# Performance work log

Measured on AMD Instinct MI355X. Metric: run time of the kernel, lower is better.

## Reference

```python
import jax, jax.numpy as jnp
import numpy as np
import math

D_MODEL = 1024
NUM_HEADS = 16
D_FF = 4096
LN_EPS = 1e-5


def _layer_norm(x, gamma, beta):
    mu = jnp.mean(x, axis=-1, keepdims=True)
    var = jnp.mean(jnp.square(x - mu), axis=-1, keepdims=True)
    return (x - mu) / jnp.sqrt(var + LN_EPS) * gamma + beta


def setup_inputs() -> dict:
    key = jax.random.key(0)
    ks = jax.random.split(key, 16)
    S, B, D, F = 2048, 2, D_MODEL, D_FF
    sc = 0.02
    inp = {
        "x": jax.random.normal(ks[0], (S, B, D), dtype=jnp.float32),
        "Wq": jax.random.normal(ks[1], (D, D), dtype=jnp.float32) * sc,
        "bq": jnp.zeros((D,), jnp.float32),
        "Wk": jax.random.normal(ks[2], (D, D), dtype=jnp.float32) * sc,
        "bk": jnp.zeros((D,), jnp.float32),
        "Wv": jax.random.normal(ks[3], (D, D), dtype=jnp.float32) * sc,
        "bv": jnp.zeros((D,), jnp.float32),
        "Wo": jax.random.normal(ks[4], (D, D), dtype=jnp.float32) * sc,
        "bo": jnp.zeros((D,), jnp.float32),
        "g1": jnp.ones((D,), jnp.float32),
        "b1": jnp.zeros((D,), jnp.float32),
        "W1": jax.random.normal(ks[5], (D, F), dtype=jnp.float32) * sc,
        "bb1": jnp.zeros((F,), jnp.float32),
        "W2": jax.random.normal(ks[6], (F, D), dtype=jnp.float32) * sc,
        "bb2": jnp.zeros((D,), jnp.float32),
        "g2": jnp.ones((D,), jnp.float32),
        "b2": jnp.zeros((D,), jnp.float32),
    }
    return inp


def reference(x, Wq, bq, Wk, bk, Wv, bv, Wo, bo, g1, b1, W1, bb1, W2, bb2, g2, b2):
    # x: [S, B, D] (seq-first, matching the torch module)
    S, B, D = x.shape
    H = NUM_HEADS
    dh = D // H

    def split_(t):  # [S, B, D] -> [B*H, S, dh]  (same as view + transpose in torch)
        return jnp.swapaxes(t.reshape(S, B * H, dh), 0, 1)

    q = split_(x @ Wq + bq)
    k = split_(x @ Wk + bk)
    v = split_(x @ Wv + bv)

    # naive bmm -> softmax -> bmm attention (full [B*H, S, S] scores)
    scores = jnp.einsum("nsd,ntd->nst", q / math.sqrt(dh), k)
    attn = jax.nn.softmax(scores, axis=-1)
    o = jnp.einsum("nst,ntd->nsd", attn, v)  # [B*H, S, dh]
    o = jnp.swapaxes(o, 0, 1).reshape(S, B, D) @ Wo + bo

    x1 = _layer_norm(x + o, g1, b1)
    ff = jax.nn.relu(x1 @ W1 + bb1) @ W2 + bb2
    return _layer_norm(x1 + ff, g2, b2)
```

## Files before the change

kernel.cpp:

```cpp
#include <hip/hip_runtime.h>
#include <hip/hip_bf16.h>
#include <cstdint>

typedef __bf16 bf16_t;
typedef __attribute__((ext_vector_type(8))) __bf16 bf16x8;
typedef __attribute__((ext_vector_type(4))) __bf16 bf16x4;
typedef __attribute__((ext_vector_type(2))) __bf16 bf16x2;
typedef __attribute__((ext_vector_type(4))) float f32x4;

#define GLOBAL_AS __attribute__((address_space(1)))
#define LDS_AS __attribute__((address_space(3)))

__device__ __forceinline__ void lds_load16(void* lds, const void* g) {
    __builtin_amdgcn_global_load_lds((GLOBAL_AS void*)g, (LDS_AS void*)lds, 16, 0, 0);
}

__global__ __launch_bounds__(256) void cast_f32_bf16(const float* __restrict__ in,
                                                     bf16_t* __restrict__ out, int n4) {
    int i = (blockIdx.x * 256 + threadIdx.x);
    if (i >= n4) return;
    float4 v = *(const float4*)(in + (size_t)i * 4);
    bf16x4 o;
    o[0] = (bf16_t)v.x; o[1] = (bf16_t)v.y; o[2] = (bf16_t)v.z; o[3] = (bf16_t)v.w;
    *(bf16x4*)(out + (size_t)i * 4) = o;
}

__global__ __launch_bounds__(256) void transpose_cast(const float* __restrict__ W,
                                                      bf16_t* __restrict__ WT,
                                                      int Kd, int Nd) {
    __shared__ float T[64][65];
    const int nbk = Kd >> 6;
    const int bk = blockIdx.x % nbk, bn = blockIdx.x / nbk;
    const int k0 = bk << 6, n0 = bn << 6;
    const int tid = threadIdx.x;
    #pragma unroll
    for (int rep = 0; rep < 4; ++rep) {
        int r = rep * 16 + (tid >> 4);
        int c = (tid & 15) * 4;
        float4 v = *(const float4*)(W + (size_t)(k0 + r) * Nd + n0 + c);
        T[r][c] = v.x; T[r][c + 1] = v.y; T[r][c + 2] = v.z; T[r][c + 3] = v.w;
    }
    __syncthreads();
    #pragma unroll
    for (int rep = 0; rep < 4; ++rep) {
        int r = rep * 16 + (tid >> 4);
        int c = (tid & 15) * 4;
        bf16x4 o;
        o[0] = (bf16_t)T[c][r]; o[1] = (bf16_t)T[c + 1][r];
        o[2] = (bf16_t)T[c + 2][r]; o[3] = (bf16_t)T[c + 3][r];
        *(bf16x4*)(WT + (size_t)(n0 + r) * Kd + k0 + c) = o;
    }
}

__global__ __launch_bounds__(256) void concat_bias(const float* a, const float* b,
                                                   const float* c, float* o) {
    int i = blockIdx.x * 256 + threadIdx.x;
    o[i] = (i < 1024) ? a[i] : (i < 2048) ? b[i - 1024] : c[i - 2048];
}

template <int OM , bool RELU>
__global__ __launch_bounds__(512, 2) void gemm256(const bf16_t* __restrict__ A,
                                                  const bf16_t* __restrict__ Bt,
                                                  const float* __restrict__ bias,
                                                  void* __restrict__ Cv,
                                                  int M, int N, int K,
                                                  int kc_len, int n_kc) {
    __shared__ alignas(16) bf16_t As[2][256 * 64];
    __shared__ alignas(16) bf16_t Bs[2][256 * 64];
    const int tid = threadIdx.x;
    const int wid = tid >> 6, lane = tid & 63;
    const int lr = lane & 15, lg = lane >> 4;
    const int wr = wid >> 2, wc = wid & 3;
    const int lrsw = (lr & 7) << 4;

    const int nbn = N >> 8;
    const int nbase = (M >> 8) * nbn;
    const int nwg = nbase * n_kc;
    int bid = blockIdx.x;
    int wg;
    if ((nwg & 7) == 0) { int q = nwg >> 3; wg = (bid & 7) * q + (bid >> 3); }
    else wg = bid;
    const int kc = wg / nbase;
    const int inner = wg - kc * nbase;
    const int bm = inner / nbn, bn = inner % nbn;

    f32x4 acc[8][4];
    #pragma unroll
    for (int i = 0; i < 8; ++i)
        #pragma unroll
        for (int j = 0; j < 4; ++j) acc[i][j] = f32x4{0.f, 0.f, 0.f, 0.f};

    const int srow = wid * 16 + (lane >> 3);
    const int colbyte = (((lane & 7) ^ (lane >> 3)) << 4);
    const char* gA = (const char*)(A + ((size_t)(bm * 256 + srow) * K + kc * kc_len)) + colbyte;
    const char* gB = (const char*)(Bt + ((size_t)(bn * 256 + srow) * K + kc * kc_len)) + colbyte;
    const size_t rs8 = (size_t)8 * K * 2;
    const size_t rs128 = (size_t)128 * K * 2;

    auto stA = [&](int b, int half, int kt) {
        char* d = (char*)As[b] + (half * 128 + wid * 16) * 128;
        const char* s = gA + (size_t)half * rs128 + (size_t)kt * 128;
        lds_load16(d, s);
        lds_load16(d + 1024, s + rs8);
    };
    auto stB = [&](int b, int half, int kt) {
        char* d = (char*)Bs[b] + (half * 128 + wid * 16) * 128;
        const char* s = gB + (size_t)half * rs128 + (size_t)kt * 128;
        lds_load16(d, s);
        lds_load16(d + 1024, s + rs8);
    };
    auto ldA = [&](int b, int m, int kk) {
        const int row = (m >> 2) * 128 + (m & 3) * 32 + wr * 16 + lr;
        return *(const bf16x8*)((const char*)As[b] + row * 128 + ((kk * 64 + lg * 16) ^ lrsw));
    };
    auto ldB = [&](int b, int n, int kk) {
        const int row = n * 64 + wc * 16 + lr;
        return *(const bf16x8*)((const char*)Bs[b] + row * 128 + ((kk * 64 + lg * 16) ^ lrsw));
    };

    const int NT = kc_len >> 6;
    stA(0, 0, 0); stB(0, 0, 0); stB(0, 1, 0); stA(0, 1, 0);
    asm volatile("s_waitcnt vmcnt(4)" ::: "memory");
    __builtin_amdgcn_s_barrier();

    bf16x8 afr[4][2], bfr[4][2];
    #pragma unroll 1
    for (int kt = 0; kt < NT; ++kt) {
        const int buf = kt & 1;
        const int ktn = (kt + 1 < NT) ? kt + 1 : kt;

        #pragma unroll
        for (int m = 0; m < 4; ++m) {
            afr[m][0] = ldA(buf, m, 0);
            afr[m][1] = ldA(buf, m, 1);
        }
        #pragma unroll
        for (int n = 0; n < 2; ++n) {
            bfr[n][0] = ldB(buf, n, 0);
            bfr[n][1] = ldB(buf, n, 1);
        }
        stA(buf ^ 1, 0, ktn);
        __builtin_amdgcn_s_barrier();
        __builtin_amdgcn_s_setprio(1);
        #pragma unroll
        for (int m = 0; m < 4; ++m)
            #pragma unroll
            for (int n = 0; n < 2; ++n) {
                acc[m][n] = __builtin_amdgcn_mfma_f32_16x16x32_bf16(afr[m][0], bfr[n][0], acc[m][n], 0, 0, 0);
                acc[m][n] = __builtin_amdgcn_mfma_f32_16x16x32_bf16(afr[m][1], bfr[n][1], acc[m][n], 0, 0, 0);
            }
        __builtin_amdgcn_s_setprio(0);
        asm volatile("s_waitcnt vmcnt(4)" ::: "memory");
        __builtin_amdgcn_s_barrier();

        #pragma unroll
        for (int n = 2; n < 4; ++n) {
            bfr[n][0] = ldB(buf, n, 0);
            bfr[n][1] = ldB(buf, n, 1);
        }
        stB(buf ^ 1, 0, ktn);
        __builtin_amdgcn_s_barrier();
        __builtin_amdgcn_s_setprio(1);
        #pragma unroll
        for (int m = 0; m < 4; ++m)
            #pragma unroll
            for (int n = 2; n < 4; ++n) {
                acc[m][n] = __builtin_amdgcn_mfma_f32_16x16x32_bf16(afr[m][0], bfr[n][0], acc[m][n], 0, 0, 0);
                acc[m][n] = __builtin_amdgcn_mfma_f32_16x16x32_bf16(afr[m][1], bfr[n][1], acc[m][n], 0, 0, 0);
            }
        __builtin_amdgcn_s_setprio(0);
        asm volatile("s_waitcnt vmcnt(4)" ::: "memory");
        __builtin_amdgcn_s_barrier();

        #pragma unroll
        for (int m = 0; m < 4; ++m) {
            afr[m][0] = ldA(buf, m + 4, 0);
            afr[m][1] = ldA(buf, m + 4, 1);
        }
        stB(buf ^ 1, 1, ktn);
        __builtin_amdgcn_s_barrier();
        __builtin_amdgcn_s_setprio(1);
        #pragma unroll
        for (int m = 0; m < 4; ++m)
            #pragma unroll
            for (int n = 0; n < 2; ++n) {
                acc[m + 4][n] = __builtin_amdgcn_mfma_f32_16x16x32_bf16(afr[m][0], bfr[n][0], acc[m + 4][n], 0, 0, 0);
                acc[m + 4][n] = __builtin_amdgcn_mfma_f32_16x16x32_bf16(afr[m][1], bfr[n][1], acc[m + 4][n], 0, 0, 0);
            }
        __builtin_amdgcn_s_setprio(0);
        __builtin_amdgcn_s_barrier();

        stA(buf ^ 1, 1, ktn);
        __builtin_amdgcn_s_barrier();
        __builtin_amdgcn_s_setprio(1);
        #pragma unroll
        for (int m = 0; m < 4; ++m)
            #pragma unroll
            for (int n = 2; n < 4; ++n) {
                acc[m + 4][n] = __builtin_amdgcn_mfma_f32_16x16x32_bf16(afr[m][0], bfr[n][0], acc[m + 4][n], 0, 0, 0);
                acc[m + 4][n] = __builtin_amdgcn_mfma_f32_16x16x32_bf16(afr[m][1], bfr[n][1], acc[m + 4][n], 0, 0, 0);
            }
        __builtin_amdgcn_s_setprio(0);
        asm volatile("s_waitcnt vmcnt(4)" ::: "memory");
        __builtin_amdgcn_s_barrier();
    }

    float* outp = (float*)Cv + (size_t)kc * M * N;
    float bv[4];
    #pragma unroll
    for (int n = 0; n < 4; ++n) {
        const int c = (bn << 8) + n * 64 + wc * 16 + lr;
        bv[n] = (bias && kc == 0) ? bias[c] : 0.f;
    }
    #pragma unroll
    for (int m = 0; m < 8; ++m) {
        const int row0 = (bm << 8) + (m >> 2) * 128 + (m & 3) * 32 + wr * 16 + (lg << 2);
        #pragma unroll
        for (int n = 0; n < 4; ++n) {
            const int c = (bn << 8) + n * 64 + wc * 16 + lr;
            #pragma unroll
            for (int j = 0; j < 4; ++j) {
                float v = acc[m][n][j] + bv[n];
                if (RELU) v = fmaxf(v, 0.f);
                if (OM == 0) ((bf16_t*)Cv)[(size_t)(row0 + j) * N + c] = (bf16_t)v;
                else         outp[(size_t)(row0 + j) * N + c] = v;
            }
        }
    }
}

__global__ __launch_bounds__(256) void reshape_qkv(const bf16_t* __restrict__ QKV,
                                                   bf16_t* __restrict__ Q,
                                                   bf16_t* __restrict__ Kh,
                                                   bf16_t* __restrict__ VT) {
    __shared__ alignas(16) bf16_t Vl[64][72];
    const int n = blockIdx.x >> 5, st = blockIdx.x & 31;
    const int b = n >> 4, h = n & 15;
    const int s0 = st << 6;
    const int tid = threadIdx.x;
    const float qscale = 0.125f * 1.4426950408889634f;

    #pragma unroll
    for (int mat = 0; mat < 2; ++mat) {
        bf16_t* dst = mat ? Kh : Q;
        #pragma unroll
        for (int rep = 0; rep < 2; ++rep) {
            int chunk = rep * 256 + tid;
            int sl = chunk >> 3, c8 = (chunk & 7) << 3;
            size_t srow = (size_t)(s0 + sl) * 2 + b;
            bf16x8 v = *(const bf16x8*)(QKV + srow * 3072 + mat * 1024 + h * 64 + c8);
            if (mat == 0) {
                #pragma unroll
                for (int e = 0; e < 8; ++e) v[e] = (bf16_t)((float)v[e] * qscale);
            }
            *(bf16x8*)(dst + ((size_t)n * 2048 + s0 + sl) * 64 + c8) = v;
        }
    }
    #pragma unroll
    for (int rep = 0; rep < 2; ++rep) {
        int chunk = rep * 256 + tid;
        int sl = chunk >> 3, c8 = (chunk & 7) << 3;
        size_t srow = (size_t)(s0 + sl) * 2 + b;
        *(bf16x8*)&Vl[sl][c8] = *(const bf16x8*)(QKV + srow * 3072 + 2048 + h * 64 + c8);
    }
    __syncthreads();
    #pragma unroll
    for (int rep = 0; rep < 2; ++rep) {
        int chunk = rep * 256 + tid;
        int d = chunk >> 3, c8 = (chunk & 7) << 3;
        bf16x8 v;
        #pragma unroll
        for (int e = 0; e < 8; ++e) v[e] = Vl[c8 + e][d];
        *(bf16x8*)(VT + ((size_t)n * 64 + d) * 2048 + s0 + c8) = v;
    }
}

__global__ __launch_bounds__(256) void attn_fwd(const bf16_t* __restrict__ Q,
                                                const bf16_t* __restrict__ K,
                                                const bf16_t* __restrict__ VT,
                                                bf16_t* __restrict__ O) {
    const int S = 2048;
    const int n = blockIdx.x >> 5;
    const int qt = blockIdx.x & 31;
    const int q0 = qt << 6;
    const int tid = threadIdx.x, wid = tid >> 6, lane = tid & 63;
    const int lr = lane & 15, lg = lane >> 4;
    const int lrsw = (lr & 7) << 4;

    __shared__ alignas(16) bf16_t Ks[2][64 * 64];
    __shared__ alignas(16) bf16_t Vs[2][64 * 64];
    __shared__ alignas(16) bf16_t Ps[4][16 * 64];

    char* pbs = (char*)&Ps[wid][0];

    const bf16_t* Qrow = Q + ((size_t)n * S + q0 + wid * 16 + lr) * 64;
    const bf16x8 qf0 = *(const bf16x8*)(Qrow + lg * 8);
    const bf16x8 qf1 = *(const bf16x8*)(Qrow + 32 + lg * 8);

    const int colbyte = (((lane & 7) ^ (lane >> 3)) << 4);
    const char* ksrc0 = (const char*)(K + ((size_t)n * S + wid * 16 + (lane >> 3)) * 64) + colbyte;
    const char* ksrc1 = ksrc0 + (size_t)8 * 128;
    const char* vsrc0 = (const char*)(VT + ((size_t)n * 64 + wid * 16 + (lane >> 3)) * S) + colbyte;
    const char* vsrc1 = vsrc0 + (size_t)8 * S * 2;

    auto stage = [&](int b, int t0) {
        lds_load16((char*)Ks[b] + wid * 2048,        ksrc0 + (size_t)t0 * 128);
        lds_load16((char*)Ks[b] + wid * 2048 + 1024, ksrc1 + (size_t)t0 * 128);
        lds_load16((char*)Vs[b] + wid * 2048,        vsrc0 + (size_t)t0 * 2);
        lds_load16((char*)Vs[b] + wid * 2048 + 1024, vsrc1 + (size_t)t0 * 2);
    };

    f32x4 oacc[4];
    #pragma unroll
    for (int i = 0; i < 4; ++i) oacc[i] = f32x4{0.f, 0.f, 0.f, 0.f};
    float m_run = -1e30f, l_part = 0.f;

    stage(0, 0);
    __syncthreads();
    int buf = 0;

    #pragma unroll 1
    for (int t0 = 0; t0 < S; t0 += 64) {
        if (t0 + 64 < S) stage(buf ^ 1, t0 + 64);
        const char* kb = (char*)Ks[buf];
        const char* vb = (char*)Vs[buf];

        f32x4 sw[4];
        #pragma unroll
        for (int tc = 0; tc < 4; ++tc) {
            const char* krow = kb + (tc * 16 + lr) * 128;
            bf16x8 kf0 = *(const bf16x8*)(krow + ((lg * 16) ^ lrsw));
            bf16x8 kf1 = *(const bf16x8*)(krow + ((64 + lg * 16) ^ lrsw));
            f32x4 z = f32x4{0.f, 0.f, 0.f, 0.f};
            z = __builtin_amdgcn_mfma_f32_16x16x32_bf16(kf0, qf0, z, 0, 0, 0);
            z = __builtin_amdgcn_mfma_f32_16x16x32_bf16(kf1, qf1, z, 0, 0, 0);
            sw[tc] = z;
        }

        float smax = sw[0][0];
        #pragma unroll
        for (int tc = 0; tc < 4; ++tc)
            #pragma unroll
            for (int j = 0; j < 4; ++j) smax = fmaxf(smax, sw[tc][j]);
        if (!__all(smax - m_run <= 8.0f)) {
            float mr = fmaxf(smax, __shfl_xor(smax, 16));
            mr = fmaxf(mr, __shfl_xor(mr, 32));
            const float mn = fmaxf(m_run, mr);
            const float sc = __builtin_amdgcn_exp2f(m_run - mn);
            m_run = mn;
            l_part *= sc;
            #pragma unroll
            for (int vc = 0; vc < 4; ++vc)
                #pragma unroll
                for (int j = 0; j < 4; ++j) oacc[vc][j] *= sc;
        }
        float rsum = 0.f;
        #pragma unroll
        for (int tc = 0; tc < 4; ++tc)
            #pragma unroll
            for (int j = 0; j < 4; ++j) {
                float p = __builtin_amdgcn_exp2f(sw[tc][j] - m_run);
                sw[tc][j] = p;
                rsum += p;
            }
        l_part += rsum;

        #pragma unroll
        for (int tc = 0; tc < 4; ++tc)
            #pragma unroll
            for (int hh = 0; hh < 2; ++hh) {
                bf16x2 pr;
                pr[0] = (bf16_t)sw[tc][2 * hh];
                pr[1] = (bf16_t)sw[tc][2 * hh + 1];
                *(bf16x2*)(pbs + lr * 128 + ((tc * 32 + lg * 8 + hh * 4) ^ lrsw)) = pr;
            }
        bf16x8 pB0 = *(const bf16x8*)(pbs + lr * 128 + ((lg * 16) ^ lrsw));
        bf16x8 pB1 = *(const bf16x8*)(pbs + lr * 128 + ((64 + lg * 16) ^ lrsw));

        #pragma unroll
        for (int vc = 0; vc < 4; ++vc) {
            const char* vrow = vb + (vc * 16 + lr) * 128;
            bf16x8 vf0 = *(const bf16x8*)(vrow + ((lg * 16) ^ lrsw));
            bf16x8 vf1 = *(const bf16x8*)(vrow + ((64 + lg * 16) ^ lrsw));
            oacc[vc] = __builtin_amdgcn_mfma_f32_16x16x32_bf16(vf0, pB0, oacc[vc], 0, 0, 0);
            oacc[vc] = __builtin_amdgcn_mfma_f32_16x16x32_bf16(vf1, pB1, oacc[vc], 0, 0, 0);
        }
        __syncthreads();
        buf ^= 1;
    }

    float l = l_part + __shfl_xor(l_part, 16);
    l += __shfl_xor(l, 32);
    const int b = n >> 4, h = n & 15;
    const float inv = 1.0f / l;
    const size_t tok = (size_t)(q0 + wid * 16 + lr) * 2 + b;
    #pragma unroll
    for (int vc = 0; vc < 4; ++vc) {
        bf16x4 o4;
        #pragma unroll
        for (int j = 0; j < 4; ++j) o4[j] = (bf16_t)(oacc[vc][j] * inv);
        *(bf16x4*)(O + tok * 1024 + h * 64 + vc * 16 + lg * 4) = o4;
    }
}

template <int P>
__global__ __launch_bounds__(256) void ln_res(const float* __restrict__ X,
                                              const float* __restrict__ Y,
                                              const float* __restrict__ g,
                                              const float* __restrict__ be,
                                              float* __restrict__ outf,
                                              bf16_t* __restrict__ outb) {
    const int row = blockIdx.x, tid = threadIdx.x;
    const size_t base = (size_t)row * 1024 + tid * 4;
    const size_t pstride = (size_t)4096 * 1024;
    float4 xv = *(const float4*)(X + base);
    float v0 = xv.x, v1 = xv.y, v2 = xv.z, v3 = xv.w;
    #pragma unroll
    for (int p = 0; p < P; ++p) {
        float4 yv = *(const float4*)(Y + p * pstride + base);
        v0 += yv.x; v1 += yv.y; v2 += yv.z; v3 += yv.w;
    }
    float s = v0 + v1 + v2 + v3;
    float sq = v0 * v0 + v1 * v1 + v2 * v2 + v3 * v3;
    #pragma unroll
    for (int m = 1; m < 64; m <<= 1) {
        s += __shfl_xor(s, m);
        sq += __shfl_xor(sq, m);
    }
    __shared__ float rs[4], rq[4];
    const int wid = tid >> 6;
    if ((tid & 63) == 0) { rs[wid] = s; rq[wid] = sq; }
    __syncthreads();
    s = rs[0] + rs[1] + rs[2] + rs[3];
    sq = rq[0] + rq[1] + rq[2] + rq[3];
    const float mu = s * (1.f / 1024.f);
    const float var = sq * (1.f / 1024.f) - mu * mu;
    const float rstd = rsqrtf(var + 1e-5f);
    float4 gv = *(const float4*)(g + tid * 4);
    float4 bv = *(const float4*)(be + tid * 4);
    float o0 = (v0 - mu) * rstd * gv.x + bv.x;
    float o1 = (v1 - mu) * rstd * gv.y + bv.y;
    float o2 = (v2 - mu) * rstd * gv.z + bv.z;
    float o3 = (v3 - mu) * rstd * gv.w + bv.w;
    float4 ov = {o0, o1, o2, o3};
    *(float4*)(outf + base) = ov;
    if (outb) {
        bf16x4 ob;
        ob[0] = (bf16_t)o0; ob[1] = (bf16_t)o1; ob[2] = (bf16_t)o2; ob[3] = (bf16_t)o3;
        *(bf16x4*)(outb + base) = ob;
    }
}

extern "C" void kernel_launch(void* const* d_in, const int* in_sizes, int n_in,
                              void* d_out, int out_size, void* d_ws, size_t ws_size,
                              hipStream_t stream) {
    (void)in_sizes; (void)n_in; (void)out_size; (void)ws_size;
    const float* x   = (const float*)d_in[0];
    const float* Wq  = (const float*)d_in[1];
    const float* bq  = (const float*)d_in[2];
    const float* Wk  = (const float*)d_in[3];
    const float* bk  = (const float*)d_in[4];
    const float* Wv  = (const float*)d_in[5];
    const float* bv  = (const float*)d_in[6];
    const float* Wo  = (const float*)d_in[7];
    const float* bo  = (const float*)d_in[8];
    const float* g1  = (const float*)d_in[9];
    const float* b1  = (const float*)d_in[10];
    const float* W1  = (const float*)d_in[11];
    const float* bb1 = (const float*)d_in[12];
    const float* W2  = (const float*)d_in[13];
    const float* bb2 = (const float*)d_in[14];
    const float* g2  = (const float*)d_in[15];
    const float* b2  = (const float*)d_in[16];
    float* out = (float*)d_out;

    char* ws = (char*)d_ws;
    const size_t MB = 1ull << 20;
    bf16_t* xb    = (bf16_t*)(ws + 0);
    bf16_t* WqkvT = (bf16_t*)(ws + 8 * MB);
    bf16_t* WoT   = (bf16_t*)(ws + 14 * MB);
    bf16_t* W1T   = (bf16_t*)(ws + 16 * MB);
    bf16_t* W2T   = (bf16_t*)(ws + 24 * MB);
    float*  qkvb  = (float*)(ws + 32 * MB);
    bf16_t* QKV   = (bf16_t*)(ws + 33 * MB);
    float*  WoP   = (float*)(ws + 33 * MB);
    float*  W2P   = (float*)(ws + 33 * MB);
    bf16_t* Qh    = (bf16_t*)(ws + 57 * MB);
    bf16_t* Kh    = (bf16_t*)(ws + 65 * MB);
    bf16_t* VTh   = (bf16_t*)(ws + 73 * MB);
    float*  x1f   = (float*)(ws + 97 * MB);
    bf16_t* x1b   = (bf16_t*)(ws + 113 * MB);
    bf16_t* Hff   = (bf16_t*)(ws + 121 * MB);
    bf16_t* Otok  = (bf16_t*)(ws + 153 * MB);

    cast_f32_bf16<<<4096, 256, 0, stream>>>(x, xb, 1024 * 1024);
    transpose_cast<<<256, 256, 0, stream>>>(Wq, WqkvT, 1024, 1024);
    transpose_cast<<<256, 256, 0, stream>>>(Wk, WqkvT + 1024 * 1024, 1024, 1024);
    transpose_cast<<<256, 256, 0, stream>>>(Wv, WqkvT + 2048 * 1024, 1024, 1024);
    transpose_cast<<<256, 256, 0, stream>>>(Wo, WoT, 1024, 1024);
    transpose_cast<<<1024, 256, 0, stream>>>(W1, W1T, 1024, 4096);
    transpose_cast<<<1024, 256, 0, stream>>>(W2, W2T, 4096, 1024);
    concat_bias<<<12, 256, 0, stream>>>(bq, bk, bv, qkvb);

    gemm256<0, false><<<192, 512, 0, stream>>>(xb, WqkvT, qkvb, QKV, 4096, 3072, 1024, 1024, 1);
    reshape_qkv<<<1024, 256, 0, stream>>>(QKV, Qh, Kh, VTh);
    attn_fwd<<<1024, 256, 0, stream>>>(Qh, Kh, VTh, Otok);
    gemm256<1, false><<<256, 512, 0, stream>>>(Otok, WoT, bo, WoP, 4096, 1024, 1024, 256, 4);
    ln_res<4><<<4096, 256, 0, stream>>>(x, WoP, g1, b1, x1f, x1b);

    gemm256<0, true><<<256, 512, 0, stream>>>(x1b, W1T, bb1, Hff, 4096, 4096, 1024, 1024, 1);
    gemm256<1, false><<<256, 512, 0, stream>>>(Hff, W2T, bb2, W2P, 4096, 1024, 4096, 1024, 4);
    ln_res<4><<<4096, 256, 0, stream>>>(x1f, W2P, g2, b2, out, nullptr);
}
```

Baseline: 271.5 us.

## Store split-K GEMM partials in bf16 and relax attention loop barriers

The Wo and W2 split-K GEMMs now write their four partial sums as bf16 instead of fp32 (new OM==2 path), and ln_res reads bf16 partials. This halves the partial-buffer write and read traffic between the GEMMs and the residual LayerNorm, at the cost of rounding each partial to bf16 before it is summed. The attention loop swaps __syncthreads for explicit vmcnt waits plus s_barrier, so the next K/V tile's loads stay in flight while the current tile is computed. The row-max reduction is also rebuilt as a tree to shorten the dependency chain. Workspace offsets are moved to fit the new buffer sizes.

```diff
diff --git a/kernel.cpp b/kernel.cpp
--- a/kernel.cpp
+++ b/kernel.cpp
@@ -58,7 +58,7 @@
     o[i] = (i < 1024) ? a[i] : (i < 2048) ? b[i - 1024] : c[i - 2048];
 }
 
-template <int OM , bool RELU>
+template <int OM, bool RELU>
 __global__ __launch_bounds__(512, 2) void gemm256(const bf16_t* __restrict__ A,
                                                   const bf16_t* __restrict__ Bt,
                                                   const float* __restrict__ bias,
@@ -205,7 +205,8 @@
         __builtin_amdgcn_s_barrier();
     }
 
-    float* outp = (float*)Cv + (size_t)kc * M * N;
+    float* outf = (float*)Cv + (size_t)kc * M * N;
+    bf16_t* outb = (bf16_t*)Cv + (size_t)kc * M * N;
     float bv[4];
     #pragma unroll
     for (int n = 0; n < 4; ++n) {
@@ -222,8 +223,9 @@
             for (int j = 0; j < 4; ++j) {
                 float v = acc[m][n][j] + bv[n];
                 if (RELU) v = fmaxf(v, 0.f);
-                if (OM == 0) ((bf16_t*)Cv)[(size_t)(row0 + j) * N + c] = (bf16_t)v;
-                else         outp[(size_t)(row0 + j) * N + c] = v;
+                if (OM == 0)      ((bf16_t*)Cv)[(size_t)(row0 + j) * N + c] = (bf16_t)v;
+                else if (OM == 1) outf[(size_t)(row0 + j) * N + c] = v;
+                else              outb[(size_t)(row0 + j) * N + c] = (bf16_t)v;
             }
         }
     }
@@ -316,12 +318,18 @@
     float m_run = -1e30f, l_part = 0.f;
 
     stage(0, 0);
-    __syncthreads();
     int buf = 0;
 
     #pragma unroll 1
     for (int t0 = 0; t0 < S; t0 += 64) {
-        if (t0 + 64 < S) stage(buf ^ 1, t0 + 64);
+        if (t0 + 64 < S) {
+            stage(buf ^ 1, t0 + 64);
+            asm volatile("s_waitcnt vmcnt(4)" ::: "memory");
+        } else {
+            asm volatile("s_waitcnt vmcnt(0)" ::: "memory");
+        }
+        __builtin_amdgcn_s_barrier();
+
         const char* kb = (char*)Ks[buf];
         const char* vb = (char*)Vs[buf];
 
@@ -337,11 +345,12 @@
             sw[tc] = z;
         }
 
-        float smax = sw[0][0];
-        #pragma unroll
-        for (int tc = 0; tc < 4; ++tc)
-            #pragma unroll
-            for (int j = 0; j < 4; ++j) smax = fmaxf(smax, sw[tc][j]);
+        float ma = fmaxf(fmaxf(sw[0][0], sw[0][1]), sw[0][2]);
+        float mb = fmaxf(fmaxf(sw[0][3], sw[1][0]), sw[1][1]);
+        float mc = fmaxf(fmaxf(sw[1][2], sw[1][3]), sw[2][0]);
+        float md = fmaxf(fmaxf(sw[2][1], sw[2][2]), sw[2][3]);
+        float me = fmaxf(fmaxf(sw[3][0], sw[3][1]), sw[3][2]);
+        float smax = fmaxf(fmaxf(fmaxf(ma, mb), fmaxf(mc, md)), fmaxf(me, sw[3][3]));
         if (!__all(smax - m_run <= 8.0f)) {
             float mr = fmaxf(smax, __shfl_xor(smax, 16));
             mr = fmaxf(mr, __shfl_xor(mr, 32));
@@ -385,7 +394,7 @@
             oacc[vc] = __builtin_amdgcn_mfma_f32_16x16x32_bf16(vf0, pB0, oacc[vc], 0, 0, 0);
             oacc[vc] = __builtin_amdgcn_mfma_f32_16x16x32_bf16(vf1, pB1, oacc[vc], 0, 0, 0);
         }
-        __syncthreads();
+        __builtin_amdgcn_s_barrier();
         buf ^= 1;
     }
 
@@ -405,7 +414,7 @@
 
 template <int P>
 __global__ __launch_bounds__(256) void ln_res(const float* __restrict__ X,
-                                              const float* __restrict__ Y,
+                                              const bf16_t* __restrict__ Y,
                                               const float* __restrict__ g,
                                               const float* __restrict__ be,
                                               float* __restrict__ outf,
@@ -417,8 +426,8 @@
     float v0 = xv.x, v1 = xv.y, v2 = xv.z, v3 = xv.w;
     #pragma unroll
     for (int p = 0; p < P; ++p) {
-        float4 yv = *(const float4*)(Y + p * pstride + base);
-        v0 += yv.x; v1 += yv.y; v2 += yv.z; v3 += yv.w;
+        bf16x4 yv = *(const bf16x4*)(Y + p * pstride + base);
+        v0 += (float)yv[0]; v1 += (float)yv[1]; v2 += (float)yv[2]; v3 += (float)yv[3];
     }
     float s = v0 + v1 + v2 + v3;
     float sq = v0 * v0 + v1 * v1 + v2 * v2 + v3 * v3;
@@ -483,11 +492,11 @@
     bf16_t* W2T   = (bf16_t*)(ws + 24 * MB);
     float*  qkvb  = (float*)(ws + 32 * MB);
     bf16_t* QKV   = (bf16_t*)(ws + 33 * MB);
-    float*  WoP   = (float*)(ws + 33 * MB);
-    float*  W2P   = (float*)(ws + 33 * MB);
-    bf16_t* Qh    = (bf16_t*)(ws + 57 * MB);
-    bf16_t* Kh    = (bf16_t*)(ws + 65 * MB);
-    bf16_t* VTh   = (bf16_t*)(ws + 73 * MB);
+    bf16_t* WoP   = (bf16_t*)(ws + 33 * MB);
+    bf16_t* W2P   = (bf16_t*)(ws + 33 * MB);
+    bf16_t* Qh    = (bf16_t*)(ws + 65 * MB);
+    bf16_t* Kh    = (bf16_t*)(ws + 73 * MB);
+    bf16_t* VTh   = (bf16_t*)(ws + 81 * MB);
     float*  x1f   = (float*)(ws + 97 * MB);
     bf16_t* x1b   = (bf16_t*)(ws + 113 * MB);
     bf16_t* Hff   = (bf16_t*)(ws + 121 * MB);
@@ -505,10 +514,10 @@
     gemm256<0, false><<<192, 512, 0, stream>>>(xb, WqkvT, qkvb, QKV, 4096, 3072, 1024, 1024, 1);
     reshape_qkv<<<1024, 256, 0, stream>>>(QKV, Qh, Kh, VTh);
     attn_fwd<<<1024, 256, 0, stream>>>(Qh, Kh, VTh, Otok);
-    gemm256<1, false><<<256, 512, 0, stream>>>(Otok, WoT, bo, WoP, 4096, 1024, 1024, 256, 4);
+    gemm256<2, false><<<256, 512, 0, stream>>>(Otok, WoT, bo, WoP, 4096, 1024, 1024, 256, 4);
     ln_res<4><<<4096, 256, 0, stream>>>(x, WoP, g1, b1, x1f, x1b);
 
     gemm256<0, true><<<256, 512, 0, stream>>>(x1b, W1T, bb1, Hff, 4096, 4096, 1024, 1024, 1);
-    gemm256<1, false><<<256, 512, 0, stream>>>(Hff, W2T, bb2, W2P, 4096, 1024, 4096, 1024, 4);
+    gemm256<2, false><<<256, 512, 0, stream>>>(Hff, W2T, bb2, W2P, 4096, 1024, 4096, 1024, 4);
     ln_res<4><<<4096, 256, 0, stream>>>(x1f, W2P, g2, b2, out, nullptr);
 }
```

Result: faster. 259.6 us (-4.4%).
